# Kernel tuning notes

Hardware: AMD Instinct MI355X
Metric: run time of the kernel (lower is better)

Reference implementation:

```python
import jax, jax.numpy as jnp
import numpy as np

N_NODES = 50000
N_EDGES = 800000
D_IN = 128
NUM_GRAPHS = 1000
H1, H2, H3 = 32, 64, 128  # hidden_dim, output_dim, output_dim*2 (nheads=1, concat)
NCLASSES = 2
EPS = 1e-5


def setup_inputs() -> dict:
    key = jax.random.key(0)
    ks = jax.random.split(key, 32)
    g = lambda i, shape, scale=1.0: (jax.random.normal(ks[i], shape, dtype=jnp.float32) * scale)
    inp = {
        "x": g(0, (N_NODES, D_IN)),
        "edge_weigth": jax.random.uniform(ks[1], (N_EDGES,), dtype=jnp.float32),
        "edge_index": jax.random.randint(ks[2], (2, N_EDGES), 0, N_NODES, dtype=jnp.int32),
        "batch": jnp.sort(jax.random.randint(ks[3], (N_NODES,), 0, NUM_GRAPHS, dtype=jnp.int32)),
    }
    # GAT layer params (heads=1): W [in,out], att_src/att_dst [out], bias [out]
    inp.update({
        "W1": g(4, (D_IN, H1), 0.1), "as1": g(5, (H1,), 0.1), "ad1": g(6, (H1,), 0.1), "b1": jnp.zeros((H1,), jnp.float32),
        "W2": g(7, (H1, H2), 0.1), "as2": g(8, (H2,), 0.1), "ad2": g(9, (H2,), 0.1), "b2": jnp.zeros((H2,), jnp.float32),
        "W3": g(10, (H2, H3), 0.1), "as3": g(11, (H3,), 0.1), "ad3": g(12, (H3,), 0.1), "b3": jnp.zeros((H3,), jnp.float32),
        "g1": jnp.ones((H1,), jnp.float32), "be1": jnp.zeros((H1,), jnp.float32),
        "g2": jnp.ones((H2,), jnp.float32), "be2": jnp.zeros((H2,), jnp.float32),
        "g3": jnp.ones((H3,), jnp.float32), "be3": jnp.zeros((H3,), jnp.float32),
        "fc1_w": g(13, (H3, H3), 0.1), "fc1_b": jnp.zeros((H3,), jnp.float32),
        "fc2_w": g(14, (H3, H2), 0.1), "fc2_b": jnp.zeros((H2,), jnp.float32),
        "fc3_w": g(15, (H2, NCLASSES), 0.1), "fc3_b": jnp.zeros((NCLASSES,), jnp.float32),
    })
    return inp


def _gat(x, src, dst, W, a_s, a_d, b):
    # PyG GATConv, heads=1, self-loops already appended to src/dst.
    h = x @ W                                   # [N, C]
    e_src = h @ a_s                             # [N]
    e_dst = h @ a_d                             # [N]
    e = jax.nn.leaky_relu(e_src[src] + e_dst[dst], 0.2)   # [E+N] edge logits
    e_max = jax.ops.segment_max(e, dst, num_segments=N_NODES)
    ee = jnp.exp(e - e_max[dst])
    denom = jax.ops.segment_sum(ee, dst, num_segments=N_NODES)
    alpha = ee / (denom[dst] + 1e-16)           # segment softmax over incoming edges
    out = jax.ops.segment_sum(h[src] * alpha[:, None], dst, num_segments=N_NODES)
    return out + b


def _bn(x, gamma, beta):
    # training-mode BatchNorm1d over node dim
    mu = jnp.mean(x, axis=0)
    var = jnp.var(x, axis=0)
    return (x - mu) * jax.lax.rsqrt(var + EPS) * gamma + beta


def reference(x, edge_weigth, W1, as1, ad1, b1, W2, as2, ad2, b2, W3, as3, ad3, b3,
              g1, be1, g2, be2, g3, be3, fc1_w, fc1_b, fc2_w, fc2_b, fc3_w, fc3_b,
              edge_index, batch):
    loop = jnp.arange(N_NODES, dtype=edge_index.dtype)
    src = jnp.concatenate([edge_index[0], loop])
    dst = jnp.concatenate([edge_index[1], loop])
    lr = lambda v: jax.nn.leaky_relu(v, 0.01)
    h = lr(_bn(_gat(x, src, dst, W1, as1, ad1, b1), g1, be1))
    h = lr(_bn(_gat(h, src, dst, W2, as2, ad2, b2), g2, be2))
    h = lr(_bn(_gat(h, src, dst, W3, as3, ad3, b3), g3, be3))
    pool = jax.ops.segment_sum(h, batch, num_segments=NUM_GRAPHS)  # global_add_pool
    o = lr(pool @ fc1_w + fc1_b)
    o = lr(o @ fc2_w + fc2_b)
    o = lr(o @ fc3_w + fc3_b)
    return o
```

## Files before the change

kernel.cpp:

```cpp
#include <hip/hip_runtime.h>
#include <hip/hip_bf16.h>

#define N_NODES_C 50000
#define N_EDGES_C 800000
#define E_TOT (N_EDGES_C + N_NODES_C)
#define NUM_GRAPHS_C 1000
#define EPS_C 1e-5f
#define SH 8
#define TILE_M 128
#define KC 32
#define NB_BUCK ((N_NODES_C + 127) / 128)
#define CAPB 4096
#define EPB 2048
#define EPT 8

static __device__ __forceinline__ float lrelu(float v, float slope) {
  return v >= 0.f ? v : slope * v;
}
static __device__ __forceinline__ float bf2f(unsigned short u) {
  return __uint_as_float((unsigned)u << 16);
}
static __device__ __forceinline__ unsigned short f2bf(float f) {
  __hip_bfloat16 b = __float2bfloat16(f);
  return *reinterpret_cast<unsigned short*>(&b);
}

__global__ void bucket_scatter(const int* __restrict__ ei, const int* __restrict__ batch,
                               unsigned* __restrict__ temp, int* __restrict__ gcnt,
                               int* __restrict__ gdeg) {
  __shared__ int cnt[NB_BUCK], base[NB_BUCK];
  int t = threadIdx.x;
  for (int b = t; b < NB_BUCK; b += 256) cnt[b] = 0;
  __syncthreads();
  int e0 = blockIdx.x * EPB;
  int bks[EPT], rks[EPT];
  unsigned pks[EPT];
#pragma unroll
  for (int k = 0; k < EPT; ++k) {
    int i = e0 + k * 256 + t;
    bks[k] = -1;
    if (i < E_TOT) {
      int s, d;
      if (i < N_EDGES_C) { s = ei[i]; d = ei[N_EDGES_C + i]; }
      else { s = d = i - N_EDGES_C; }
      int b = d >> 7;
      bks[k] = b;
      pks[k] = ((unsigned)s << 7) | (unsigned)(d & 127);
      rks[k] = atomicAdd(&cnt[b], 1);
    }
  }
  __syncthreads();
  for (int b = t; b < NB_BUCK; b += 256) {
    int c = cnt[b];
    base[b] = c ? atomicAdd(&gcnt[b], c) : 0;
  }
  int gid = blockIdx.x * 256 + t;
  if (gid < N_NODES_C) atomicAdd(&gdeg[batch[gid]], 1);
  __syncthreads();
#pragma unroll
  for (int k = 0; k < EPT; ++k) {
    if (bks[k] >= 0)
      temp[(size_t)bks[k] * CAPB + base[bks[k]] + rks[k]] = pks[k];
  }
}

static __device__ __forceinline__ int block_excl_scan_1024(int v, int* wsum) {
  int t = threadIdx.x, lane = t & 63, wid = t >> 6;
  int x = v;
#pragma unroll
  for (int off = 1; off < 64; off <<= 1) {
    int y = __shfl_up(x, off, 64);
    if (lane >= off) x += y;
  }
  if (lane == 63) wsum[wid] = x;
  __syncthreads();
  if (t < 16) {
    int w = wsum[t];
#pragma unroll
    for (int off = 1; off < 16; off <<= 1) {
      int y = __shfl_up(w, off, 64);
      if (t >= off) w += y;
    }
    wsum[t] = w;
  }
  __syncthreads();
  return (wid ? wsum[wid - 1] : 0) + (x - v);
}

__global__ void tiny_scan(const int* __restrict__ gcnt, int* __restrict__ gbase,
                          const int* __restrict__ gdeg, int* __restrict__ gptr,
                          int* __restrict__ rowptr) {
  __shared__ int wsum[16];
  int t = threadIdx.x;
  int v1 = (t < NB_BUCK) ? gcnt[t] : 0;
  int e1 = block_excl_scan_1024(v1, wsum);
  if (t < NB_BUCK) gbase[t] = e1;
  __syncthreads();
  int v2 = (t < NUM_GRAPHS_C) ? gdeg[t] : 0;
  int e2 = block_excl_scan_1024(v2, wsum);
  if (t < NUM_GRAPHS_C) gptr[t] = e2;
  if (t == 0) { gptr[NUM_GRAPHS_C] = N_NODES_C; rowptr[N_NODES_C] = E_TOT; }
}

__global__ void bucket_build(const unsigned* __restrict__ temp, const int* __restrict__ gcnt,
                             const int* __restrict__ gbase, int* __restrict__ rowptr,
                             int* __restrict__ csr_src) {
  __shared__ int hist[128], lscan[128], cur[128];
  __shared__ int stage[CAPB];
  int b = blockIdx.x, t = threadIdx.x;
  int cnt = gcnt[b], gb = gbase[b];
  int nloc = min(128, N_NODES_C - b * 128);
  if (t < 128) hist[t] = 0;
  __syncthreads();
  const unsigned* tp = temp + (size_t)b * CAPB;
  for (int i = t; i < cnt; i += 256) atomicAdd(&hist[tp[i] & 127], 1);
  __syncthreads();
  if (t < 128) lscan[t] = hist[t];
  __syncthreads();
  for (int off = 1; off < 128; off <<= 1) {
    int add = (t < 128 && t >= off) ? lscan[t - off] : 0;
    __syncthreads();
    if (t < 128) lscan[t] += add;
    __syncthreads();
  }
  if (t < 128) {
    int excl = lscan[t] - hist[t];
    if (t < nloc) rowptr[b * 128 + t] = gb + excl;
    hist[t] = excl;
    cur[t] = 0;
  }
  __syncthreads();
  for (int i = t; i < cnt; i += 256) {
    unsigned w = tp[i];
    int dl = w & 127;
    int pos = hist[dl] + atomicAdd(&cur[dl], 1);
    stage[pos] = (int)(w >> 7);
  }
  __syncthreads();
  for (int i = t; i < cnt; i += 256) csr_src[gb + i] = stage[i];
}

template<int CIN, int COUT, int OCG, bool BN>
__global__ __launch_bounds__(256) void gemm_tiled(
    const float* __restrict__ x, const float* __restrict__ W,
    const float* __restrict__ a_s, const float* __restrict__ a_d,
    const double* __restrict__ sums, const float* __restrict__ gamma,
    const float* __restrict__ beta,
    __hip_bfloat16* __restrict__ hb, float* __restrict__ es, float* __restrict__ ed) {
  constexpr int NG = 256 / OCG;
  constexpr int Nn = COUT / OCG;
  constexpr int Mn = TILE_M / NG;
  constexpr int XPITCH = TILE_M + 4;
  static_assert(Mn == 4 || Mn == 8, "");
  static_assert(Nn == 4 || Nn == 8, "");

  __shared__ float sW[CIN * COUT];
  __shared__ float sxT[KC * XPITCH];
  __shared__ float sA[COUT], sD[COUT];
  __shared__ float sbn[BN ? 2 * CIN : 1];

  int t = threadIdx.x;
  if (BN && t < CIN) {
    double s = 0.0, q = 0.0;
    for (int k = 0; k < SH; ++k) { s += sums[k * 2 * CIN + t]; q += sums[k * 2 * CIN + CIN + t]; }
    double mu = s / N_NODES_C;
    double var = q / N_NODES_C - mu * mu;
    float sc = gamma[t] * rsqrtf((float)var + EPS_C);
    sbn[t] = sc;
    sbn[CIN + t] = beta[t] - (float)mu * sc;
  }
  if (t < COUT) { sA[t] = a_s[t]; sD[t] = a_d[t]; }
  for (int i = t; i < CIN * COUT; i += 256) sW[i] = W[i];

  int og = t % OCG;
  int ng = t / OCG;
  int node0 = blockIdx.x * TILE_M;

  float acc[Mn][Nn];
#pragma unroll
  for (int mi = 0; mi < Mn; ++mi)
#pragma unroll
    for (int ni = 0; ni < Nn; ++ni) acc[mi][ni] = 0.f;

  for (int kc0 = 0; kc0 < CIN; kc0 += KC) {
    __syncthreads();
    for (int idx = t; idx < TILE_M * KC; idx += 256) {
      int nl = idx / KC, cl = idx % KC;
      int n = node0 + nl;
      float v = (n < N_NODES_C) ? x[(size_t)n * CIN + kc0 + cl] : 0.f;
      if (BN) { int c = kc0 + cl; v = lrelu(v * sbn[c] + sbn[CIN + c], 0.01f); }
      sxT[cl * XPITCH + nl] = v;
    }
    __syncthreads();
#pragma unroll 4
    for (int k = 0; k < KC; ++k) {
      float ax[Mn], bw[Nn];
      *reinterpret_cast<float4*>(&ax[0]) =
          *reinterpret_cast<const float4*>(&sxT[k * XPITCH + ng * Mn]);
      if constexpr (Mn == 8)
        *reinterpret_cast<float4*>(&ax[4]) =
            *reinterpret_cast<const float4*>(&sxT[k * XPITCH + ng * Mn + 4]);
      *reinterpret_cast<float4*>(&bw[0]) =
          *reinterpret_cast<const float4*>(&sW[(kc0 + k) * COUT + og * Nn]);
      if constexpr (Nn == 8)
        *reinterpret_cast<float4*>(&bw[4]) =
            *reinterpret_cast<const float4*>(&sW[(kc0 + k) * COUT + og * Nn + 4]);
#pragma unroll
      for (int mi = 0; mi < Mn; ++mi)
#pragma unroll
        for (int ni = 0; ni < Nn; ++ni) acc[mi][ni] += ax[mi] * bw[ni];
    }
  }

#pragma unroll
  for (int mi = 0; mi < Mn; ++mi) {
    int n = node0 + ng * Mn + mi;
    bool act = (n < N_NODES_C);
    if (act) {
      unsigned short hv[Nn];
#pragma unroll
      for (int ni = 0; ni < Nn; ++ni) hv[ni] = f2bf(acc[mi][ni]);
      if constexpr (Nn == 4) {
        uint2 u;
        u.x = (unsigned)hv[0] | ((unsigned)hv[1] << 16);
        u.y = (unsigned)hv[2] | ((unsigned)hv[3] << 16);
        *reinterpret_cast<uint2*>(&hb[(size_t)n * COUT + og * Nn]) = u;
      } else {
        uint4 u;
        u.x = (unsigned)hv[0] | ((unsigned)hv[1] << 16);
        u.y = (unsigned)hv[2] | ((unsigned)hv[3] << 16);
        u.z = (unsigned)hv[4] | ((unsigned)hv[5] << 16);
        u.w = (unsigned)hv[6] | ((unsigned)hv[7] << 16);
        *reinterpret_cast<uint4*>(&hb[(size_t)n * COUT + og * Nn]) = u;
      }
    }
    float ps = 0.f, pd = 0.f;
#pragma unroll
    for (int ni = 0; ni < Nn; ++ni) {
      int oc = og * Nn + ni;
      ps += acc[mi][ni] * sA[oc];
      pd += acc[mi][ni] * sD[oc];
    }
#pragma unroll
    for (int off = 1; off < OCG; off <<= 1) {
      ps += __shfl_xor(ps, off, 64);
      pd += __shfl_xor(pd, off, 64);
    }
    if (act && og == 0) { es[n] = ps; ed[n] = pd; }
  }
}

template<int C>
__global__ void gat_aggregate(const int* __restrict__ rowptr, const int* __restrict__ csr_src,
                              const float* __restrict__ es, const float* __restrict__ ed,
                              const char* __restrict__ hb, float* __restrict__ agg) {
  constexpr int LPE = C / 4;
  constexpr int EPW = 64 / LPE;
  __shared__ uint2 sp[4][64];
  int t = threadIdx.x;
  int lane = t & 63;
  int wid = t >> 6;
  int node = (blockIdx.x * 256 + t) >> 6;
  if (node >= N_NODES_C) return;
  int r0 = rowptr[node];
  int deg = rowptr[node + 1] - r0;
  float edv = ed[node];

  if (deg <= 64) {
    int srcj = 0; float e = -1e30f;
    if (lane < deg) { srcj = csr_src[r0 + lane]; e = lrelu(es[srcj] + edv, 0.2f); }
    float m = e;
#pragma unroll
    for (int off = 32; off; off >>= 1) m = fmaxf(m, __shfl_xor(m, off, 64));
    float ee = (lane < deg) ? __expf(e - m) : 0.f;
    float ssum = ee;
#pragma unroll
    for (int off = 32; off; off >>= 1) ssum += __shfl_xor(ssum, off, 64);
    float alpha = ee / (ssum + 1e-16f);
    sp[wid][lane] = make_uint2((lane < deg) ? (unsigned)srcj * (C * 2) : 0u,
                               (lane < deg) ? __float_as_uint(alpha) : 0u);
    int sub = lane / LPE;
    int cl = lane % LPE;
    int nit = (deg + EPW - 1) / EPW;
    float a0 = 0.f, a1 = 0.f, a2 = 0.f, a3 = 0.f;
#pragma unroll 4
    for (int j = 0; j < nit; ++j) {
      uint2 p = sp[wid][j * EPW + sub];
      float al = __uint_as_float(p.y);
      ushort4 u = *reinterpret_cast<const ushort4*>(hb + p.x + cl * 8);
      a0 += al * bf2f(u.x);
      a1 += al * bf2f(u.y);
      a2 += al * bf2f(u.z);
      a3 += al * bf2f(u.w);
    }
#pragma unroll
    for (int off = 32; off >= LPE; off >>= 1) {
      a0 += __shfl_xor(a0, off, 64);
      a1 += __shfl_xor(a1, off, 64);
      a2 += __shfl_xor(a2, off, 64);
      a3 += __shfl_xor(a3, off, 64);
    }
    if (lane < LPE) {
      float4 o; o.x = a0; o.y = a1; o.z = a2; o.w = a3;
      *reinterpret_cast<float4*>(&agg[(size_t)node * C + lane * 4]) = o;
    }
  } else {
    const unsigned short* hbu = (const unsigned short*)hb;
    float m = -1e30f;
    for (int j = lane; j < deg; j += 64)
      m = fmaxf(m, lrelu(es[csr_src[r0 + j]] + edv, 0.2f));
#pragma unroll
    for (int off = 32; off; off >>= 1) m = fmaxf(m, __shfl_xor(m, off, 64));
    float ssum = 0.f;
    for (int j = lane; j < deg; j += 64)
      ssum += __expf(lrelu(es[csr_src[r0 + j]] + edv, 0.2f) - m);
#pragma unroll
    for (int off = 32; off; off >>= 1) ssum += __shfl_xor(ssum, off, 64);
    float inv = 1.f / (ssum + 1e-16f);
    float acc0 = 0.f, acc1 = 0.f;
    for (int base = 0; base < deg; base += 64) {
      int j = base + lane; int srcj = 0; float al = 0.f;
      if (j < deg) { srcj = csr_src[r0 + j]; al = __expf(lrelu(es[srcj] + edv, 0.2f) - m) * inv; }
      int cnt = min(64, deg - base);
      for (int tt = 0; tt < cnt; ++tt) {
        int sj = __shfl(srcj, tt, 64);
        float al_t = __shfl(al, tt, 64);
        if constexpr (C == 128) {
          ushort2 u = *reinterpret_cast<const ushort2*>(&hbu[(size_t)sj * 128 + lane * 2]);
          acc0 += al_t * bf2f(u.x);
          acc1 += al_t * bf2f(u.y);
        } else if constexpr (C == 64) {
          acc0 += al_t * bf2f(hbu[(size_t)sj * 64 + lane]);
        } else {
          if (lane < C) acc0 += al_t * bf2f(hbu[(size_t)sj * C + lane]);
        }
      }
    }
    if constexpr (C == 128) {
      float2 o; o.x = acc0; o.y = acc1;
      *reinterpret_cast<float2*>(&agg[(size_t)node * 128 + lane * 2]) = o;
    } else if constexpr (C == 64) {
      agg[(size_t)node * 64 + lane] = acc0;
    } else {
      if (lane < C) agg[(size_t)node * C + lane] = acc0;
    }
  }
}

template<int C>
__global__ void bn_stats(const float* __restrict__ x, double* __restrict__ sums, int n_nodes) {
  constexpr int TPC = 256 / C;
  constexpr int ROWS = 128;
  int c = threadIdx.x % C;
  int rs = threadIdx.x / C;
  int r0 = blockIdx.x * ROWS;
  int rend = min(r0 + ROWS, n_nodes);
  double s = 0.0, q = 0.0;
  for (int r = r0 + rs; r < rend; r += TPC) {
    float v = x[(size_t)r * C + c];
    s += v; q += (double)v * (double)v;
  }
  __shared__ double ss[256], sq[256];
  ss[threadIdx.x] = s; sq[threadIdx.x] = q;
  __syncthreads();
#pragma unroll
  for (int off = 128; off >= C; off >>= 1) {
    if (threadIdx.x < off) {
      ss[threadIdx.x] += ss[threadIdx.x + off];
      sq[threadIdx.x] += sq[threadIdx.x + off];
    }
    __syncthreads();
  }
  if (threadIdx.x < C) {
    double* dst = sums + (size_t)(blockIdx.x & (SH - 1)) * (2 * C);
    unsafeAtomicAdd(&dst[c], ss[threadIdx.x]);
    unsafeAtomicAdd(&dst[C + c], sq[threadIdx.x]);
  }
}

__global__ void poolfc_kernel(const float* __restrict__ agg3, const int* __restrict__ gptr,
                              const double* __restrict__ sums, const float* __restrict__ gamma,
                              const float* __restrict__ beta,
                              const float* __restrict__ fc1w, const float* __restrict__ fc1b,
                              const float* __restrict__ fc2w, const float* __restrict__ fc2b,
                              const float* __restrict__ fc3w, const float* __restrict__ fc3b,
                              float* __restrict__ out) {
  __shared__ float sc[128], sh[128];
  __shared__ float row[128], buf[128];
  int t = threadIdx.x;
  {
    double s = 0.0, q = 0.0;
    for (int k = 0; k < SH; ++k) { s += sums[k * 256 + t]; q += sums[k * 256 + 128 + t]; }
    double mu = s / N_NODES_C;
    double var = q / N_NODES_C - mu * mu;
    float scale = gamma[t] * rsqrtf((float)var + EPS_C);
    sc[t] = scale;
    sh[t] = beta[t] - (float)mu * scale;
  }
  __syncthreads();
  int g = blockIdx.x;
  int n0 = gptr[g], n1 = gptr[g + 1];
  float acc = 0.f;
  float scale = sc[t], shift = sh[t];
  for (int n = n0; n < n1; ++n)
    acc += lrelu(agg3[(size_t)n * 128 + t] * scale + shift, 0.01f);
  row[t] = acc;
  __syncthreads();
  {
    float s = fc1b[t];
#pragma unroll 8
    for (int k = 0; k < 128; ++k) s += row[k] * fc1w[k * 128 + t];
    buf[t] = lrelu(s, 0.01f);
  }
  __syncthreads();
  if (t < 64) {
    float s = fc2b[t];
#pragma unroll 8
    for (int k = 0; k < 128; ++k) s += buf[k] * fc2w[k * 64 + t];
    row[t] = lrelu(s, 0.01f);
  }
  __syncthreads();
  if (t < 2) {
    float s = fc3b[t];
#pragma unroll 8
    for (int k = 0; k < 64; ++k) s += row[k] * fc3w[k * 2 + t];
    out[(size_t)g * 2 + t] = lrelu(s, 0.01f);
  }
}

extern "C" void kernel_launch(void* const* d_in, const int* in_sizes, int n_in,
                              void* d_out, int out_size, void* d_ws, size_t ws_size,
                              hipStream_t stream) {
  const float* x    = (const float*)d_in[0];
  const int* ei     = (const int*)d_in[2];
  const int* batch  = (const int*)d_in[3];
  const float* W1   = (const float*)d_in[4];
  const float* as1  = (const float*)d_in[5];
  const float* ad1  = (const float*)d_in[6];
  const float* W2   = (const float*)d_in[8];
  const float* as2  = (const float*)d_in[9];
  const float* ad2  = (const float*)d_in[10];
  const float* W3   = (const float*)d_in[12];
  const float* as3  = (const float*)d_in[13];
  const float* ad3  = (const float*)d_in[14];
  const float* g1   = (const float*)d_in[16];
  const float* be1  = (const float*)d_in[17];
  const float* g2   = (const float*)d_in[18];
  const float* be2  = (const float*)d_in[19];
  const float* g3   = (const float*)d_in[20];
  const float* be3  = (const float*)d_in[21];
  const float* fc1w = (const float*)d_in[22];
  const float* fc1b = (const float*)d_in[23];
  const float* fc2w = (const float*)d_in[24];
  const float* fc2b = (const float*)d_in[25];
  const float* fc3w = (const float*)d_in[26];
  const float* fc3b = (const float*)d_in[27];
  float* out = (float*)d_out;

  char* ws = (char*)d_ws;
  size_t off = 0;
  auto alloc = [&](size_t bytes) { size_t o = off; off += (bytes + 255) & ~(size_t)255; return o; };

  size_t o_gcnt  = alloc((size_t)NB_BUCK * 4);
  size_t o_gdeg  = alloc((size_t)NUM_GRAPHS_C * 4);
  size_t o_sum1  = alloc((size_t)SH * 2 * 32 * 8);
  size_t o_sum2  = alloc((size_t)SH * 2 * 64 * 8);
  size_t o_sum3  = alloc((size_t)SH * 2 * 128 * 8);
  size_t zero_end = off;
  size_t o_gbase = alloc((size_t)NB_BUCK * 4);
  size_t o_gptr  = alloc((size_t)(NUM_GRAPHS_C + 1) * 4);
  size_t o_rowp  = alloc((size_t)(N_NODES_C + 1) * 4);
  size_t o_temp  = alloc((size_t)NB_BUCK * CAPB * 4);
  size_t o_csr   = alloc((size_t)E_TOT * 4);
  size_t o_hb    = alloc((size_t)N_NODES_C * 128 * 2);
  size_t o_es    = alloc((size_t)N_NODES_C * 4);
  size_t o_ed    = alloc((size_t)N_NODES_C * 4);
  size_t o_agg1  = alloc((size_t)N_NODES_C * 32 * 4);
  size_t o_agg2  = alloc((size_t)N_NODES_C * 64 * 4);
  size_t o_agg3  = alloc((size_t)N_NODES_C * 128 * 4);

  hipMemsetAsync(ws, 0, zero_end, stream);

  int* gcnt    = (int*)(ws + o_gcnt);
  int* gdeg    = (int*)(ws + o_gdeg);
  int* gbase   = (int*)(ws + o_gbase);
  int* gptr    = (int*)(ws + o_gptr);
  int* rowptr  = (int*)(ws + o_rowp);
  unsigned* temp = (unsigned*)(ws + o_temp);
  int* csr     = (int*)(ws + o_csr);
  __hip_bfloat16* hb = (__hip_bfloat16*)(ws + o_hb);
  const char* hbc = (const char*)(ws + o_hb);
  float* es    = (float*)(ws + o_es);
  float* ed    = (float*)(ws + o_ed);
  float* agg1  = (float*)(ws + o_agg1);
  float* agg2  = (float*)(ws + o_agg2);
  float* agg3  = (float*)(ws + o_agg3);
  double* sum1 = (double*)(ws + o_sum1);
  double* sum2 = (double*)(ws + o_sum2);
  double* sum3 = (double*)(ws + o_sum3);

  const int GB = (N_NODES_C + TILE_M - 1) / TILE_M;

  bucket_scatter<<<(E_TOT + EPB - 1) / EPB, 256, 0, stream>>>(ei, batch, temp, gcnt, gdeg);
  tiny_scan<<<1, 1024, 0, stream>>>(gcnt, gbase, gdeg, gptr, rowptr);
  bucket_build<<<NB_BUCK, 256, 0, stream>>>(temp, gcnt, gbase, rowptr, csr);

  gemm_tiled<128, 32, 8, false><<<GB, 256, 0, stream>>>(
      x, W1, as1, ad1, nullptr, nullptr, nullptr, hb, es, ed);
  gat_aggregate<32><<<N_NODES_C / 4, 256, 0, stream>>>(rowptr, csr, es, ed, hbc, agg1);
  bn_stats<32><<<(N_NODES_C + 127) / 128, 256, 0, stream>>>(agg1, sum1, N_NODES_C);

  gemm_tiled<32, 64, 16, true><<<GB, 256, 0, stream>>>(
      agg1, W2, as2, ad2, sum1, g1, be1, hb, es, ed);
  gat_aggregate<64><<<N_NODES_C / 4, 256, 0, stream>>>(rowptr, csr, es, ed, hbc, agg2);
  bn_stats<64><<<(N_NODES_C + 127) / 128, 256, 0, stream>>>(agg2, sum2, N_NODES_C);

  gemm_tiled<64, 128, 16, true><<<GB, 256, 0, stream>>>(
      agg2, W3, as3, ad3, sum2, g2, be2, hb, es, ed);
  gat_aggregate<128><<<N_NODES_C / 4, 256, 0, stream>>>(rowptr, csr, es, ed, hbc, agg3);
  bn_stats<128><<<(N_NODES_C + 127) / 128, 256, 0, stream>>>(agg3, sum3, N_NODES_C);

  poolfc_kernel<<<NUM_GRAPHS_C, 128, 0, stream>>>(agg3, gptr, sum3, g3, be3,
                                                  fc1w, fc1b, fc2w, fc2b, fc3w, fc3b, out);
}
```

Measured before the change: 260.2 us.

## Double-buffer x tiles via register prefetch in tiled GEMM kernel

Restructures the node-feature GEMM to double-buffer the transposed x tile in shared memory. The next K-chunk is prefetched into registers while the current chunk is computed, which hides global load latency and drops one barrier per chunk. It also unrolls the weight copy into batched loads and makes the K-chunk size a template parameter (16 for the third layer), at the cost of more registers and shared memory. A stray no-op read expression is left in write_regs.

```diff
diff --git a/kernel.cpp b/kernel.cpp
--- a/kernel.cpp
+++ b/kernel.cpp
@@ -8,7 +8,6 @@
 #define EPS_C 1e-5f
 #define SH 8
 #define TILE_M 128
-#define KC 32
 #define NB_BUCK ((N_NODES_C + 127) / 128)
 #define CAPB 4096
 #define EPB 2048
@@ -140,7 +139,7 @@
   for (int i = t; i < cnt; i += 256) csr_src[gb + i] = stage[i];
 }
 
-template<int CIN, int COUT, int OCG, bool BN>
+template<int CIN, int COUT, int OCG, int KCT, bool BN>
 __global__ __launch_bounds__(256) void gemm_tiled(
     const float* __restrict__ x, const float* __restrict__ W,
     const float* __restrict__ a_s, const float* __restrict__ a_d,
@@ -151,11 +150,14 @@
   constexpr int Nn = COUT / OCG;
   constexpr int Mn = TILE_M / NG;
   constexpr int XPITCH = TILE_M + 4;
+  constexpr int NCH = CIN / KCT;
+  constexpr int PFN = TILE_M * KCT / 256;
+  constexpr int NLS = 256 / KCT;
   static_assert(Mn == 4 || Mn == 8, "");
   static_assert(Nn == 4 || Nn == 8, "");
 
   __shared__ float sW[CIN * COUT];
-  __shared__ float sxT[KC * XPITCH];
+  __shared__ float sxT[2][KCT * XPITCH];
   __shared__ float sA[COUT], sD[COUT];
   __shared__ float sbn[BN ? 2 * CIN : 1];
 
@@ -170,11 +172,44 @@
     sbn[CIN + t] = beta[t] - (float)mu * sc;
   }
   if (t < COUT) { sA[t] = a_s[t]; sD[t] = a_d[t]; }
-  for (int i = t; i < CIN * COUT; i += 256) sW[i] = W[i];
+  {
+    constexpr int WTOT = CIN * COUT / 256;
+#pragma unroll
+    for (int b0 = 0; b0 < WTOT; b0 += 16) {
+      constexpr int B = (WTOT < 16) ? WTOT : 16;
+      float wt[B];
+#pragma unroll
+      for (int j = 0; j < B; ++j) wt[j] = W[(b0 + j) * 256 + t];
+#pragma unroll
+      for (int j = 0; j < B; ++j) sW[(b0 + j) * 256 + t] = wt[j];
+    }
+  }
 
   int og = t % OCG;
   int ng = t / OCG;
   int node0 = blockIdx.x * TILE_M;
+  int cl = t % KCT;
+  int nlb = t / KCT;
+
+  float pf[PFN];
+  auto load_regs = [&](int kc0) {
+#pragma unroll
+    for (int j = 0; j < PFN; ++j) {
+      int n = node0 + nlb + NLS * j;
+      pf[j] = (n < N_NODES_C) ? x[(size_t)n * CIN + kc0 + cl] : 0.f;
+    }
+  };
+  auto write_regs = [&](float* dst, int kc0) {
+    float scl = 1.f, shf = 0.f;
+    if (BN) { scl = sbn[kc0 + cl]; shf = sbn[CIN + kc0 + cl]; }
+#pragma unroll
+    for (int j = 0; j < PFN; ++j) {
+      float v = pf[j];
+      if (BN) v = lrelu(v * scl + shf, 0.01f);
+      dst[cl * XPITCH + nlb + NLS * j];
+      dst[cl * XPITCH + nlb + NLS * j] = v;
+    }
+  };
 
   float acc[Mn][Nn];
 #pragma unroll
@@ -182,33 +217,36 @@
 #pragma unroll
     for (int ni = 0; ni < Nn; ++ni) acc[mi][ni] = 0.f;
 
-  for (int kc0 = 0; kc0 < CIN; kc0 += KC) {
-    __syncthreads();
-    for (int idx = t; idx < TILE_M * KC; idx += 256) {
-      int nl = idx / KC, cl = idx % KC;
-      int n = node0 + nl;
-      float v = (n < N_NODES_C) ? x[(size_t)n * CIN + kc0 + cl] : 0.f;
-      if (BN) { int c = kc0 + cl; v = lrelu(v * sbn[c] + sbn[CIN + c], 0.01f); }
-      sxT[cl * XPITCH + nl] = v;
-    }
-    __syncthreads();
+  load_regs(0);
+  __syncthreads();
+  write_regs(sxT[0], 0);
+  __syncthreads();
+
+  for (int c = 0; c < NCH; ++c) {
+    const float* cur = sxT[c & 1];
+    int kcn = (c + 1) * KCT;
+    if (kcn < CIN) load_regs(kcn);
 #pragma unroll 4
-    for (int k = 0; k < KC; ++k) {
+    for (int k = 0; k < KCT; ++k) {
       float ax[Mn], bw[Nn];
       *reinterpret_cast<float4*>(&ax[0]) =
-          *reinterpret_cast<const float4*>(&sxT[k * XPITCH + ng * Mn]);
+          *reinterpret_cast<const float4*>(&cur[k * XPITCH + ng * Mn]);
       if constexpr (Mn == 8)
         *reinterpret_cast<float4*>(&ax[4]) =
-            *reinterpret_cast<const float4*>(&sxT[k * XPITCH + ng * Mn + 4]);
+            *reinterpret_cast<const float4*>(&cur[k * XPITCH + ng * Mn + 4]);
       *reinterpret_cast<float4*>(&bw[0]) =
-          *reinterpret_cast<const float4*>(&sW[(kc0 + k) * COUT + og * Nn]);
+          *reinterpret_cast<const float4*>(&sW[(c * KCT + k) * COUT + og * Nn]);
       if constexpr (Nn == 8)
         *reinterpret_cast<float4*>(&bw[4]) =
-            *reinterpret_cast<const float4*>(&sW[(kc0 + k) * COUT + og * Nn + 4]);
+            *reinterpret_cast<const float4*>(&sW[(c * KCT + k) * COUT + og * Nn + 4]);
 #pragma unroll
       for (int mi = 0; mi < Mn; ++mi)
 #pragma unroll
         for (int ni = 0; ni < Nn; ++ni) acc[mi][ni] += ax[mi] * bw[ni];
+    }
+    if (kcn < CIN) {
+      write_regs((float*)sxT[(c + 1) & 1], kcn);
+      __syncthreads();
     }
   }
 
@@ -505,17 +543,17 @@
   tiny_scan<<<1, 1024, 0, stream>>>(gcnt, gbase, gdeg, gptr, rowptr);
   bucket_build<<<NB_BUCK, 256, 0, stream>>>(temp, gcnt, gbase, rowptr, csr);
 
-  gemm_tiled<128, 32, 8, false><<<GB, 256, 0, stream>>>(
+  gemm_tiled<128, 32, 8, 32, false><<<GB, 256, 0, stream>>>(
       x, W1, as1, ad1, nullptr, nullptr, nullptr, hb, es, ed);
   gat_aggregate<32><<<N_NODES_C / 4, 256, 0, stream>>>(rowptr, csr, es, ed, hbc, agg1);
   bn_stats<32><<<(N_NODES_C + 127) / 128, 256, 0, stream>>>(agg1, sum1, N_NODES_C);
 
-  gemm_tiled<32, 64, 16, true><<<GB, 256, 0, stream>>>(
+  gemm_tiled<32, 64, 16, 32, true><<<GB, 256, 0, stream>>>(
       agg1, W2, as2, ad2, sum1, g1, be1, hb, es, ed);
   gat_aggregate<64><<<N_NODES_C / 4, 256, 0, stream>>>(rowptr, csr, es, ed, hbc, agg2);
   bn_stats<64><<<(N_NODES_C + 127) / 128, 256, 0, stream>>>(agg2, sum2, N_NODES_C);
 
-  gemm_tiled<64, 128, 16, true><<<GB, 256, 0, stream>>>(
+  gemm_tiled<64, 128, 16, 16, true><<<GB, 256, 0, stream>>>(
       agg2, W3, as3, ad3, sum2, g2, be2, hb, es, ed);
   gat_aggregate<128><<<N_NODES_C / 4, 256, 0, stream>>>(rowptr, csr, es, ed, hbc, agg3);
   bn_stats<128><<<(N_NODES_C + 127) / 128, 256, 0, stream>>>(agg3, sum3, N_NODES_C);
```

Measured after the change: 238.8 us (median of 2 runs). 1.09x faster.
